# Kernel optimization log

Hardware: AMD Instinct MI355X
Metric: run time of the kernel (lower is better)

The kernel has to match this reference:

```python
import jax, jax.numpy as jnp
import numpy as np

KA = 2  # kernel_att == stride

def _unfold2(t):
    # torch nn.Unfold(kernel=2, stride=2, pad=0): [B,C,H,W] -> [B, C, 4, L], L=(H/2)*(W/2)
    B, C, H, W = t.shape
    t = t.reshape(B, C, H // KA, KA, W // KA, KA).transpose(0, 1, 3, 5, 2, 4)
    return t.reshape(B, C, KA * KA, (H // KA) * (W // KA))

def _fold2(t, H, W):
    # inverse of _unfold2 (non-overlapping): [B, C, 4, L] -> [B, C, H, W]
    B, C, _, L = t.shape
    t = t.reshape(B, C, KA, KA, H // KA, W // KA).transpose(0, 1, 4, 2, 5, 3)
    return t.reshape(B, C, H, W)

def setup_inputs() -> dict:
    key = jax.random.key(0)
    ks = jax.random.split(key, 5)
    b, c, m, h, w = 4, 16, 8, 64, 64
    O = 64
    return {
        "x": jax.random.normal(ks[0], (b, c, m, h, w), jnp.float32),
        "w_q": jax.random.normal(ks[1], (O, m), jnp.float32) * 0.1,
        "w_k": jax.random.normal(ks[2], (O, m), jnp.float32) * 0.1,
        "w_v": jax.random.normal(ks[3], (O, m), jnp.float32) * 0.1,
        "w_p": jax.random.normal(ks[4], (2,), jnp.float32) * 0.1,
    }

def reference(x, w_q, w_k, w_v, w_p):
    b, c, m, h, w = x.shape
    O = w_q.shape[0]
    # res = AdaptiveAvgPool3d((1, dim, dim)) with h==w==dim -> mean over m only
    res = x.mean(axis=2, keepdims=True)            # [b, c, 1, h, w]
    xf = x.reshape(b * c, m, h, w)
    # 1x1 convs (bias-free) are channel matmuls
    q = jnp.einsum('om,bmhw->bohw', w_q, xf)       # [b*c, O, h, w]
    k = jnp.einsum('om,bmhw->bohw', w_k, xf)
    v = jnp.einsum('om,bmhw->bohw', w_v, xf)
    # relative position map pe = conv_p(position(h, w)) -> [1,1,h,w]
    loc_w = jnp.linspace(-1.0, 1.0, w)[None, :]    # varies along W
    loc_h = jnp.linspace(-1.0, 1.0, h)[:, None]    # varies along H
    pe = (w_p[0] * loc_w + w_p[1] * loc_h)[None, None]  # [1,1,h,w]
    q5 = q.reshape(b, c, O, h, w).transpose(0, 2, 1, 3, 4)  # permuted: [b, O, c, h, w]
    k5 = k.reshape(b, c, O, h, w) + pe             # pe broadcast over trailing (h,w)
    v5 = v.reshape(b, c, O, h, w)
    scaling = float(h) ** (-0.5)
    B = b * O
    q_att = (q5 * scaling).reshape(B, c, h, w)
    # NB: torch code views the UNpermuted [b,c,O,h,w] buffer as [b*O, c, h, w] (raw reinterpretation)
    k_att = k5.reshape(B, c, h, w)
    v_att = v5.reshape(B, c, h, w)
    uq = _unfold2(q_att)                           # [B, c, 4, L]
    uk = _unfold2(k_att) + _unfold2(pe)            # unfold_rpe broadcast: [B, c, 4, L]
    uv = _unfold2(v_att)
    # att[B,i,j,l] = sum_p q[B,i,p,l] * k[B,j,p,l]
    att = jnp.einsum('bipl,bjpl->bijl', uq, uk)    # [B, c, c, L]
    att = jax.nn.softmax(att, axis=2)
    out = jnp.einsum('bijl,bjpl->bipl', att, uv)   # [B, c, 4, L]
    out = _fold2(out, h, w)                        # [B, c, h, w]
    out = out.reshape(b, O, c, h, w).transpose(0, 2, 1, 3, 4)  # [b, c, O, h, w]
    return out + res
```

## Files before the change

kernel.cpp:

```cpp
#include <hip/hip_runtime.h>

typedef float v2f __attribute__((ext_vector_type(2)));


__global__ __launch_bounds__(256, 4) void adapt_attn(
    const float* __restrict__ x,  const float* __restrict__ wq,
    const float* __restrict__ wk, const float* __restrict__ wv,
    const float* __restrict__ wp, float* __restrict__ out)
{
    __shared__ __align__(16) float s_wk[128];
    __shared__ __align__(16) float s_wv[128];
    __shared__ v2f    s_xk[2][8][2][16];
    __shared__ float4 s_uk[2][16][16];
    __shared__ float4 s_uv[2][16][16];

    const int tid = threadIdx.x;
    const int bid = blockIdx.x;
    const int tg = bid & 31;
    const int o  = (bid >> 5) & 63;
    const int bb = bid >> 11;
    const int r = o & 3, qch = o >> 2;

    const v2f* __restrict__ x2 = (const v2f*)x;

    v2f s1v[2];
    #pragma unroll
    for (int it = 0; it < 2; it++) {
        const int idx = it * 256 + tid;
        const int p = idx & 15, row = (idx >> 4) & 1, m = (idx >> 5) & 7, t = idx >> 8;
        const int tile = tg * 2 + t;
        const int y0 = (tile >> 1) << 1, ww0 = (tile & 1) << 4;
        s1v[it] = x2[((bb * 16 + qch) * 8 + m) * 2048 + (y0 + row) * 32 + ww0 + p];
    }

    float wkv_k = 0.f, wkv_v = 0.f;
    if (tid < 128) {
        wkv_k = wk[(r << 7) + tid];
        wkv_v = wv[(r << 7) + tid];
    }

    const int p3 = tid & 15, ig = (tid >> 4) & 7, t3 = tid >> 7;
    const int tile3 = tg * 2 + t3;
    const int y03 = (tile3 >> 1) << 1, ww03 = (tile3 & 1) << 4;
    const int sp = y03 * 32 + ww03 + p3;

    v2f qa0[8], qb0[8], qa1[8], qb1[8];
    {
        const int bq0 = (bb * 16 + ig * 2) * 16384 + sp;
        const int bq1 = bq0 + 16384;
        #pragma unroll
        for (int m = 0; m < 8; m++) {
            qa0[m] = x2[bq0 + m * 2048];
            qb0[m] = x2[bq0 + m * 2048 + 32];
            qa1[m] = x2[bq1 + m * 2048];
            qb1[m] = x2[bq1 + m * 2048 + 32];
        }
    }

    #pragma unroll
    for (int it = 0; it < 2; it++) {
        const int idx = it * 256 + tid;
        const int p = idx & 15, row = (idx >> 4) & 1, m = (idx >> 5) & 7, t = idx >> 8;
        s_xk[t][m][row][p] = s1v[it];
    }
    if (tid < 128) {
        s_wk[tid] = wkv_k;
        s_wv[tid] = wkv_v;
    }

    float wqr[8];
    #pragma unroll
    for (int m = 0; m < 8; m++) wqr[m] = 0.125f * wq[(o << 3) + m];

    v2f uqa0 = {0.f, 0.f}, uqb0 = {0.f, 0.f}, rsa0 = {0.f, 0.f}, rsb0 = {0.f, 0.f};
    v2f uqa1 = {0.f, 0.f}, uqb1 = {0.f, 0.f}, rsa1 = {0.f, 0.f}, rsb1 = {0.f, 0.f};
    #pragma unroll
    for (int m = 0; m < 8; m++) {
        uqa0 += qa0[m] * wqr[m];
        uqb0 += qb0[m] * wqr[m];
        rsa0 += qa0[m];
        rsb0 += qb0[m];
        uqa1 += qa1[m] * wqr[m];
        uqb1 += qb1[m] * wqr[m];
        rsa1 += qa1[m];
        rsb1 += qb1[m];
    }
    __syncthreads();

    const float wp0 = wp[0], wp1 = wp[1];
    const float step = 2.0f / 63.0f;
    #pragma unroll
    for (int it = 0; it < 2; it++) {
        const int idx = it * 256 + tid;
        const int p = idx & 15, j = (idx >> 4) & 15, t = idx >> 8;
        const int tile = tg * 2 + t;
        const int y0 = (tile >> 1) << 1, ww0 = (tile & 1) << 4;
        const int wwp = ww0 + p;
        const float lx0 = -1.0f + step * (float)(wwp << 1);
        const float lx1 = lx0 + step;
        const float ly0 = -1.0f + step * (float)y0;
        const float ly1 = ly0 + step;
        v2f ka = { 2.0f * (wp0 * lx0 + wp1 * ly0), 2.0f * (wp0 * lx1 + wp1 * ly0) };
        v2f kb = { 2.0f * (wp0 * lx0 + wp1 * ly1), 2.0f * (wp0 * lx1 + wp1 * ly1) };
        v2f va = {0.f, 0.f}, vb = {0.f, 0.f};

        float wkj[8], wvj[8];
        *(float4*)&wkj[0] = ((const float4*)s_wk)[j * 2];
        *(float4*)&wkj[4] = ((const float4*)s_wk)[j * 2 + 1];
        *(float4*)&wvj[0] = ((const float4*)s_wv)[j * 2];
        *(float4*)&wvj[4] = ((const float4*)s_wv)[j * 2 + 1];

        #pragma unroll
        for (int m = 0; m < 8; m++) {
            const v2f xa = s_xk[t][m][0][p];
            const v2f xb = s_xk[t][m][1][p];
            ka += xa * wkj[m]; kb += xb * wkj[m];
            va += xa * wvj[m]; vb += xb * wvj[m];
        }
        s_uk[t][j][p] = make_float4(ka.x, ka.y, kb.x, kb.y);
        s_uv[t][j][p] = make_float4(va.x, va.y, vb.x, vb.y);
    }
    __syncthreads();

    {
        v2f oa0 = {0.f, 0.f}, ob0 = {0.f, 0.f};
        v2f oa1 = {0.f, 0.f}, ob1 = {0.f, 0.f};
        float sum0 = 0.f, sum1 = 0.f;

        #pragma unroll
        for (int j = 0; j < 16; j++) {
            const float4 k4 = s_uk[t3][j][p3];
            const float4 v4 = s_uv[t3][j][p3];
            const v2f ka = {k4.x, k4.y}, kb = {k4.z, k4.w};
            const v2f va = {v4.x, v4.y}, vb = {v4.z, v4.w};

            v2f t0 = uqa0 * ka;
            t0 += uqb0 * kb;
            const float e0 = __expf(t0.x + t0.y);
            sum0 += e0;
            oa0 += va * e0;
            ob0 += vb * e0;

            v2f t1 = uqa1 * ka;
            t1 += uqb1 * kb;
            const float e1 = __expf(t1.x + t1.y);
            sum1 += e1;
            oa1 += va * e1;
            ob1 += vb * e1;
        }

        v2f* __restrict__ out2 = (v2f*)out;
        {
            const int i = ig * 2;
            const float rcp = 1.0f / sum0;
            const v2f outa = oa0 * rcp + rsa0 * 0.125f;
            const v2f outb = ob0 * rcp + rsb0 * 0.125f;
            const int obi = ((bb * 16 + i) * 64 + o) * 2048 + sp;
            out2[obi]      = outa;
            out2[obi + 32] = outb;
        }
        {
            const int i = ig * 2 + 1;
            const float rcp = 1.0f / sum1;
            const v2f outa = oa1 * rcp + rsa1 * 0.125f;
            const v2f outb = ob1 * rcp + rsb1 * 0.125f;
            const int obi = ((bb * 16 + i) * 64 + o) * 2048 + sp;
            out2[obi]      = outa;
            out2[obi + 32] = outb;
        }
    }
}

extern "C" void kernel_launch(void* const* d_in, const int* in_sizes, int n_in,
                              void* d_out, int out_size, void* d_ws, size_t ws_size,
                              hipStream_t stream) {
    const float* x  = (const float*)d_in[0];
    const float* wq = (const float*)d_in[1];
    const float* wk = (const float*)d_in[2];
    const float* wv = (const float*)d_in[3];
    const float* wp = (const float*)d_in[4];
    float* out = (float*)d_out;
    adapt_attn<<<dim3(8192), dim3(256), 0, stream>>>(x, wq, wk, wv, wp, out);
}
```

Before: 118.4 us.

## Use native exp2/rcp, float4 staging loads, register-held k/v weights, raise occupancy

Several changes land together. The query scale is folded with log2(e) so the softmax can use the native exp2 builtin, and the division is replaced by the hardware reciprocal. The x tile is staged with one float4 load per thread instead of two v2f loads. The k/v weights are read directly into registers, which removes the weight shared arrays. The launch bound occupancy hint rises from 4 to 8 blocks per CU, which may force register spilling, and the approximate reciprocal slightly changes precision.

```diff
diff --git a/kernel.cpp b/kernel.cpp
--- a/kernel.cpp
+++ b/kernel.cpp
@@ -3,14 +3,25 @@
 typedef float v2f __attribute__((ext_vector_type(2)));
 
 
-__global__ __launch_bounds__(256, 4) void adapt_attn(
+#if __has_builtin(__builtin_amdgcn_exp2f)
+  #define EXP_FN(x) __builtin_amdgcn_exp2f(x)
+  #define QSCALE 0.18033688011112043f
+#else
+  #define EXP_FN(x) __expf(x)
+  #define QSCALE 0.125f
+#endif
+#if __has_builtin(__builtin_amdgcn_rcpf)
+  #define RCP_FN(x) __builtin_amdgcn_rcpf(x)
+#else
+  #define RCP_FN(x) (1.0f/(x))
+#endif
+
+__global__ __launch_bounds__(256, 8) void adapt_attn(
     const float* __restrict__ x,  const float* __restrict__ wq,
     const float* __restrict__ wk, const float* __restrict__ wv,
     const float* __restrict__ wp, float* __restrict__ out)
 {
-    __shared__ __align__(16) float s_wk[128];
-    __shared__ __align__(16) float s_wv[128];
-    __shared__ v2f    s_xk[2][8][2][16];
+    __shared__ __align__(16) v2f s_xk[2][8][2][16];
     __shared__ float4 s_uk[2][16][16];
     __shared__ float4 s_uv[2][16][16];
 
@@ -21,28 +32,26 @@
     const int bb = bid >> 11;
     const int r = o & 3, qch = o >> 2;
 
-    const v2f* __restrict__ x2 = (const v2f*)x;
+    const v2f*    __restrict__ x2 = (const v2f*)x;
+    const float4* __restrict__ x4 = (const float4*)x;
 
-    v2f s1v[2];
-    #pragma unroll
-    for (int it = 0; it < 2; it++) {
-        const int idx = it * 256 + tid;
-        const int p = idx & 15, row = (idx >> 4) & 1, m = (idx >> 5) & 7, t = idx >> 8;
+    float4 s1;
+    {
+        const int f = tid & 7, row = (tid >> 3) & 1, m = (tid >> 4) & 7, t = tid >> 7;
         const int tile = tg * 2 + t;
-        const int y0 = (tile >> 1) << 1, ww0 = (tile & 1) << 4;
-        s1v[it] = x2[((bb * 16 + qch) * 8 + m) * 2048 + (y0 + row) * 32 + ww0 + p];
-    }
-
-    float wkv_k = 0.f, wkv_v = 0.f;
-    if (tid < 128) {
-        wkv_k = wk[(r << 7) + tid];
-        wkv_v = wv[(r << 7) + tid];
+        const int y0 = (tile >> 1) << 1, w8 = (tile & 1) * 8;
+        s1 = x4[((bb * 16 + qch) * 8 + m) * 1024 + (y0 + row) * 16 + w8 + f];
     }
 
     const int p3 = tid & 15, ig = (tid >> 4) & 7, t3 = tid >> 7;
     const int tile3 = tg * 2 + t3;
     const int y03 = (tile3 >> 1) << 1, ww03 = (tile3 & 1) << 4;
     const int sp = y03 * 32 + ww03 + p3;
+
+    float wqr[8];
+    #pragma unroll
+    for (int m = 0; m < 8; m++)
+        wqr[m] = QSCALE * wq[(o << 3) + m];
 
     v2f qa0[8], qb0[8], qa1[8], qb1[8];
     {
@@ -57,23 +66,8 @@
         }
     }
 
-    #pragma unroll
-    for (int it = 0; it < 2; it++) {
-        const int idx = it * 256 + tid;
-        const int p = idx & 15, row = (idx >> 4) & 1, m = (idx >> 5) & 7, t = idx >> 8;
-        s_xk[t][m][row][p] = s1v[it];
-    }
-    if (tid < 128) {
-        s_wk[tid] = wkv_k;
-        s_wv[tid] = wkv_v;
-    }
-
-    float wqr[8];
-    #pragma unroll
-    for (int m = 0; m < 8; m++) wqr[m] = 0.125f * wq[(o << 3) + m];
-
-    v2f uqa0 = {0.f, 0.f}, uqb0 = {0.f, 0.f}, rsa0 = {0.f, 0.f}, rsb0 = {0.f, 0.f};
-    v2f uqa1 = {0.f, 0.f}, uqb1 = {0.f, 0.f}, rsa1 = {0.f, 0.f}, rsb1 = {0.f, 0.f};
+    v2f uqa0 = {0.f,0.f}, uqb0 = {0.f,0.f}, rsa0 = {0.f,0.f}, rsb0 = {0.f,0.f};
+    v2f uqa1 = {0.f,0.f}, uqb1 = {0.f,0.f}, rsa1 = {0.f,0.f}, rsb1 = {0.f,0.f};
     #pragma unroll
     for (int m = 0; m < 8; m++) {
         uqa0 += qa0[m] * wqr[m];
@@ -85,17 +79,30 @@
         rsa1 += qa1[m];
         rsb1 += qb1[m];
     }
+
+    {
+        const int f = tid & 7, row = (tid >> 3) & 1, m = (tid >> 4) & 7, t = tid >> 7;
+        *(float4*)&s_xk[t][m][row][f * 2] = s1;
+    }
+
+    const int p2 = tid & 15, j2 = (tid >> 4) & 15;
+    float wkj[8], wvj[8];
+    {
+        const float4* wk4 = (const float4*)wk;
+        const float4* wv4 = (const float4*)wv;
+        const int rb = (r * 16 + j2) * 2;
+        *(float4*)&wkj[0] = wk4[rb];   *(float4*)&wkj[4] = wk4[rb + 1];
+        *(float4*)&wvj[0] = wv4[rb];   *(float4*)&wvj[4] = wv4[rb + 1];
+    }
+    const float wp0 = wp[0], wp1 = wp[1];
     __syncthreads();
 
-    const float wp0 = wp[0], wp1 = wp[1];
     const float step = 2.0f / 63.0f;
     #pragma unroll
-    for (int it = 0; it < 2; it++) {
-        const int idx = it * 256 + tid;
-        const int p = idx & 15, j = (idx >> 4) & 15, t = idx >> 8;
+    for (int t = 0; t < 2; t++) {
         const int tile = tg * 2 + t;
         const int y0 = (tile >> 1) << 1, ww0 = (tile & 1) << 4;
-        const int wwp = ww0 + p;
+        const int wwp = ww0 + p2;
         const float lx0 = -1.0f + step * (float)(wwp << 1);
         const float lx1 = lx0 + step;
         const float ly0 = -1.0f + step * (float)y0;
@@ -104,21 +111,15 @@
         v2f kb = { 2.0f * (wp0 * lx0 + wp1 * ly1), 2.0f * (wp0 * lx1 + wp1 * ly1) };
         v2f va = {0.f, 0.f}, vb = {0.f, 0.f};
 
-        float wkj[8], wvj[8];
-        *(float4*)&wkj[0] = ((const float4*)s_wk)[j * 2];
-        *(float4*)&wkj[4] = ((const float4*)s_wk)[j * 2 + 1];
-        *(float4*)&wvj[0] = ((const float4*)s_wv)[j * 2];
-        *(float4*)&wvj[4] = ((const float4*)s_wv)[j * 2 + 1];
-
         #pragma unroll
         for (int m = 0; m < 8; m++) {
-            const v2f xa = s_xk[t][m][0][p];
-            const v2f xb = s_xk[t][m][1][p];
+            const v2f xa = s_xk[t][m][0][p2];
+            const v2f xb = s_xk[t][m][1][p2];
             ka += xa * wkj[m]; kb += xb * wkj[m];
             va += xa * wvj[m]; vb += xb * wvj[m];
         }
-        s_uk[t][j][p] = make_float4(ka.x, ka.y, kb.x, kb.y);
-        s_uv[t][j][p] = make_float4(va.x, va.y, vb.x, vb.y);
+        s_uk[t][j2][p2] = make_float4(ka.x, ka.y, kb.x, kb.y);
+        s_uv[t][j2][p2] = make_float4(va.x, va.y, vb.x, vb.y);
     }
     __syncthreads();
 
@@ -136,14 +137,14 @@
 
             v2f t0 = uqa0 * ka;
             t0 += uqb0 * kb;
-            const float e0 = __expf(t0.x + t0.y);
+            const float e0 = EXP_FN(t0.x + t0.y);
             sum0 += e0;
             oa0 += va * e0;
             ob0 += vb * e0;
 
             v2f t1 = uqa1 * ka;
             t1 += uqb1 * kb;
-            const float e1 = __expf(t1.x + t1.y);
+            const float e1 = EXP_FN(t1.x + t1.y);
             sum1 += e1;
             oa1 += va * e1;
             ob1 += vb * e1;
@@ -152,7 +153,7 @@
         v2f* __restrict__ out2 = (v2f*)out;
         {
             const int i = ig * 2;
-            const float rcp = 1.0f / sum0;
+            const float rcp = RCP_FN(sum0);
             const v2f outa = oa0 * rcp + rsa0 * 0.125f;
             const v2f outb = ob0 * rcp + rsb0 * 0.125f;
             const int obi = ((bb * 16 + i) * 64 + o) * 2048 + sp;
@@ -161,7 +162,7 @@
         }
         {
             const int i = ig * 2 + 1;
-            const float rcp = 1.0f / sum1;
+            const float rcp = RCP_FN(sum1);
             const v2f outa = oa1 * rcp + rsa1 * 0.125f;
             const v2f outb = ob1 * rcp + rsb1 * 0.125f;
             const int obi = ((bb * 16 + i) * 64 + o) * 2048 + sp;
```

Result: slower. 291.5 us (+146.2%).
